# Optimization experiments

Hardware: AMD Instinct MI355X
Metric: run time of the kernel (lower is better)

The kernel has to match this reference:

```python
import jax, jax.numpy as jnp
import numpy as np


def setup_inputs() -> dict:
    key = jax.random.key(0)
    k1, k2 = jax.random.split(key)
    z = jax.random.normal(k1, (16, 256, 32, 32), dtype=jnp.float32)
    emb = jax.random.normal(k2, (8192, 256), dtype=jnp.float32)
    return {"z": z, "emb": emb}


def reference(z, emb):
    B, C, H, W = z.shape
    # [B,C,H,W] -> [B*H*W, C], distances in fp32 for precision
    z_f = jnp.transpose(z, (0, 2, 3, 1)).reshape(-1, C).astype(jnp.float32)
    e = emb.astype(jnp.float32)
    # squared-distance expansion: ||z||^2 - 2 z.e + ||e||^2  -> [N, K]
    d = (
        jnp.sum(z_f * z_f, axis=1, keepdims=True)
        - 2.0 * (z_f @ e.T)
        + jnp.sum(e * e, axis=1)[None, :]
    )
    idx = jnp.argmin(d, axis=1)  # [N]
    out = emb[idx].astype(z.dtype)  # codebook gather
    return jnp.transpose(out.reshape(B, H, W, C), (0, 3, 1, 2))
```

## Files before the change

kernel.cpp:

```cpp
#include <hip/hip_runtime.h>
#include <stdint.h>

#define NB   16
#define CD   256
#define HW   1024
#define NQ   16384
#define KCN  8192

typedef unsigned long long u64;
typedef unsigned short     u16;
using f32x4  = __attribute__((ext_vector_type(4))) float;
using bf16x8 = __attribute__((ext_vector_type(8))) __bf16;

#define ZTB_OFF  0
#define EMBB_OFF 8388608
#define EH_OFF   12582912
#define CAND_OFF 12615680

static __device__ __forceinline__ void gl_lds16(const void* g, void* l) {
  __builtin_amdgcn_global_load_lds(
      (const __attribute__((address_space(1))) void*)g,
      (__attribute__((address_space(3))) void*)l, 16, 0, 0);
}

static __device__ __forceinline__ unsigned bf16r(float x) {
  unsigned u = __float_as_uint(x);
  return (u + 0x7fffu + ((u >> 16) & 1u)) >> 16;
}

static __device__ __forceinline__ u64 umin64(u64 a, u64 b) { return a < b ? a : b; }
static __device__ __forceinline__ u64 umax64(u64 a, u64 b) { return a < b ? b : a; }

__global__ __launch_bounds__(256) void k_prep(const float* __restrict__ z,
                                              const float* __restrict__ emb,
                                              u16* __restrict__ zTb,
                                              u16* __restrict__ embB,
                                              float* __restrict__ eH) {
  const int bx = (int)blockIdx.x;
  if (bx < 1024) {
    __shared__ float tile[64][65];
    const int b   = bx >> 6;
    const int hwT = (bx >> 2) & 15;
    const int cT  = bx & 3;
    const int tx  = threadIdx.x & 63;
    const int ty  = threadIdx.x >> 6;
    const float* src = z + (size_t)(b * CD + cT * 64) * HW + hwT * 64;
#pragma unroll
    for (int i = 0; i < 16; ++i) {
      const int c_l = ty + 4 * i;
      tile[c_l][tx] = src[(size_t)c_l * HW + tx];
    }
    __syncthreads();
    const size_t dbase = (size_t)(b * HW + hwT * 64) * CD + cT * 64;
#pragma unroll
    for (int i = 0; i < 16; ++i) {
      const int hw_l = ty + 4 * i;
      zTb[dbase + (size_t)hw_l * CD + tx] = (u16)bf16r(tile[tx][hw_l]);
    }
  } else {
    const int wave = (bx - 1024) * 4 + ((int)threadIdx.x >> 6);
    const int lane = threadIdx.x & 63;
#pragma unroll
    for (int it = 0; it < 8; ++it) {
      const int row = wave * 8 + it;
      const float4 v = *(const float4*)(emb + (size_t)row * CD + lane * 4);
      uint2 pk;
      pk.x = bf16r(v.x) | (bf16r(v.y) << 16);
      pk.y = bf16r(v.z) | (bf16r(v.w) << 16);
      *(uint2*)(embB + (size_t)row * CD + lane * 4) = pk;
      float s = v.x * v.x + v.y * v.y + v.z * v.z + v.w * v.w;
#pragma unroll
      for (int off = 32; off; off >>= 1) s += __shfl_xor(s, off, 64);
      if (lane == 0) eH[row] = 0.5f * s + 1024.0f;
    }
  }
}


#define WAITV(N) asm volatile("s_waitcnt vmcnt(" #N ")" ::: "memory")
#define MEMFENCE() asm volatile("" ::: "memory")

__global__ __launch_bounds__(256, 2) void k_argmin(const u16* __restrict__ zTb,
                                                   const u16* __restrict__ embB,
                                                   const float* __restrict__ eH,
                                                   u64* __restrict__ cand) {
  __shared__ __align__(16) u16 Bs[4][128 * 64];

  const int tid  = (int)threadIdx.x;
  const int w    = tid >> 6;
  const int lane = tid & 63;
  const int l15  = lane & 15, quad = lane >> 4;
  const int q0    = (int)(blockIdx.x >> 3) * 128;
  const int split = (int)(blockIdx.x & 7);

  bf16x8 Af[2][4][2];
  {
    const char* aB = (const char*)zTb
                   + ((size_t)(q0 + w * 32 + l15) * CD + quad * 8) * 2;
#pragma unroll
    for (int i = 0; i < 2; ++i)
#pragma unroll
      for (int kc = 0; kc < 4; ++kc)
#pragma unroll
        for (int ks = 0; ks < 2; ++ks)
          Af[i][kc][ks] = *(const bf16x8*)(aB + i * 8192 + kc * 128 + ks * 64);
  }
  MEMFENCE();

  const char* bS = (const char*)embB + (size_t)split * (1024 * 512)
                 + (size_t)(w * 32 + (lane >> 3)) * 512
                 + (size_t)(((lane & 7) ^ (lane >> 3)) * 16);
  const int ldsW = w * 4096 + lane * 16;

#define STAGE(RING, NT_, KC_)                                                  \
  do {                                                                         \
    const char* _s = bS + (NT_) * 65536 + (KC_) * 128;                         \
    char* _d = (char*)Bs[RING] + ldsW;                                         \
    gl_lds16(_s,         _d);                                                  \
    gl_lds16(_s + 4096,  _d + 1024);                                           \
    gl_lds16(_s + 8192,  _d + 2048);                                           \
    gl_lds16(_s + 12288, _d + 3072);                                           \
  } while (0)

  const int bR0 = l15 * 128 + ((quad ^ (l15 & 7)) * 16);
  const int bR1 = bR0 ^ 64;

  f32x4 acc[2][8];
  float b1[8][2], b2[8][2];
  const float FMAX = __uint_as_float(0x7F7FFFFFu);
#pragma unroll
  for (int s = 0; s < 8; ++s) { b1[s][0] = b1[s][1] = FMAX; b2[s][0] = b2[s][1] = FMAX; }

  STAGE(0, 0, 0); MEMFENCE();
  STAGE(1, 0, 1); MEMFENCE();
  STAGE(2, 0, 2); MEMFENCE();

#define MFMA_INT(RING, KC_)                                                    \
  do {                                                                         \
    const char* _b = (const char*)Bs[RING];                                    \
    _Pragma("unroll")                                                          \
    for (int ks = 0; ks < 2; ++ks) {                                           \
      bf16x8 bfr[8];                                                           \
      const int _o = ks ? bR1 : bR0;                                           \
      _Pragma("unroll")                                                        \
      for (int j = 0; j < 8; ++j)                                              \
        bfr[j] = *(const bf16x8*)(_b + j * 2048 + _o);                         \
      __builtin_amdgcn_s_setprio(1);                                           \
      _Pragma("unroll")                                                        \
      for (int i = 0; i < 2; ++i)                                              \
        _Pragma("unroll")                                                      \
        for (int j = 0; j < 8; ++j)                                            \
          acc[i][j] = __builtin_amdgcn_mfma_f32_16x16x32_bf16(                 \
              Af[i][KC_][ks], bfr[j], acc[i][j], 0, 0, 0);                     \
      __builtin_amdgcn_s_setprio(0);                                           \
    }                                                                          \
  } while (0)

#define EPILOGUE(NT_)                                                          \
  do {                                                                         \
    _Pragma("unroll")                                                          \
    for (int i = 0; i < 2; ++i)                                                \
      _Pragma("unroll")                                                        \
      for (int r = 0; r < 4; ++r) {                                            \
        const int s = i * 4 + r;                                               \
        float kq[8];                                                           \
        _Pragma("unroll")                                                      \
        for (int j = 0; j < 8; ++j)                                            \
          kq[j] = __uint_as_float(                                             \
              (__float_as_uint(eh[j] - acc[i][j][r]) & ~63u)                   \
              | (unsigned)((NT_) * 8 + j));                                    \
        _Pragma("unroll")                                                      \
        for (int h = 0; h < 2; ++h) {                                          \
          const float k0 = kq[4 * h], k1 = kq[4 * h + 1];                      \
          const float k2 = kq[4 * h + 2], k3 = kq[4 * h + 3];                  \
          const float lo01 = fminf(k0, k1), hi01 = fmaxf(k0, k1);              \
          const float lo23 = fminf(k2, k3), hi23 = fmaxf(k2, k3);              \
          const float best = fminf(lo01, lo23);                                \
          const float sec  = fminf(fmaxf(lo01, lo23), fminf(hi01, hi23));      \
          b2[s][h] = fminf(fmaxf(best, b1[s][h]), fminf(sec, b2[s][h]));       \
          b1[s][h] = fminf(best, b1[s][h]);                                    \
        }                                                                      \
      }                                                                        \
  } while (0)

  float eh[8];

  for (int nt = 0; nt < 7; ++nt) {
    const int n0 = split * 1024 + nt * 128;
#pragma unroll
    for (int i = 0; i < 2; ++i)
#pragma unroll
      for (int j = 0; j < 8; ++j) acc[i][j] = f32x4{0.f, 0.f, 0.f, 0.f};

    WAITV(8); __builtin_amdgcn_s_barrier(); MEMFENCE();
    STAGE(3, nt, 3); MEMFENCE();
#pragma unroll
    for (int j = 0; j < 8; ++j) eh[j] = eH[n0 + j * 16 + l15];
    MEMFENCE();
    MFMA_INT(0, 0);
    WAITV(16); __builtin_amdgcn_s_barrier(); MEMFENCE();
    STAGE(0, nt + 1, 0); MEMFENCE();
    MFMA_INT(1, 1);
    WAITV(16); __builtin_amdgcn_s_barrier(); MEMFENCE();
    STAGE(1, nt + 1, 1); MEMFENCE();
    MFMA_INT(2, 2);
    WAITV(16); __builtin_amdgcn_s_barrier(); MEMFENCE();
    STAGE(2, nt + 1, 2); MEMFENCE();
    MFMA_INT(3, 3);

    EPILOGUE(nt);
  }

  {
    const int n0 = split * 1024 + 7 * 128;
#pragma unroll
    for (int i = 0; i < 2; ++i)
#pragma unroll
      for (int j = 0; j < 8; ++j) acc[i][j] = f32x4{0.f, 0.f, 0.f, 0.f};

    WAITV(8); __builtin_amdgcn_s_barrier(); MEMFENCE();
    STAGE(3, 7, 3); MEMFENCE();
#pragma unroll
    for (int j = 0; j < 8; ++j) eh[j] = eH[n0 + j * 16 + l15];
    MEMFENCE();
    MFMA_INT(0, 0);

    WAITV(16); __builtin_amdgcn_s_barrier(); MEMFENCE();
    MFMA_INT(1, 1);

    WAITV(12); __builtin_amdgcn_s_barrier(); MEMFENCE();
    MFMA_INT(2, 2);

    WAITV(8); __builtin_amdgcn_s_barrier(); MEMFENCE();
    MFMA_INT(3, 3);

    EPILOGUE(7);
  }
#undef STAGE
#undef MFMA_INT
#undef EPILOGUE

  const int wh = w >> 1;
#pragma unroll
  for (int s = 0; s < 8; ++s) {
#pragma unroll
    for (int h = 0; h < 2; ++h) {
      u64 x1 = ((u64)__float_as_uint(b1[s][h]) << 32) | (unsigned)l15;
      u64 x2 = ((u64)__float_as_uint(b2[s][h]) << 32) | (unsigned)l15;
#pragma unroll
      for (int off = 1; off < 16; off <<= 1) {
        const u64 o1 = __shfl_xor(x1, off, 64);
        const u64 o2 = __shfl_xor(x2, off, 64);
        const u64 lo = umin64(x1, o1);
        const u64 hi = umax64(x1, o1);
        x1 = lo;
        x2 = umin64(hi, umin64(x2, o2));
      }
      if (l15 == 0) {
        const int i = s >> 2, r = s & 3;
        const int q = q0 + w * 32 + i * 16 + quad * 4 + r;
        const unsigned kb1 = (unsigned)(x1 >> 32), kb2 = (unsigned)(x2 >> 32);
        const int n1 = split * 1024 + (int)((kb1 >> 3) & 7) * 128
                       + (int)(kb1 & 7) * 16 + (int)(x1 & 15);
        const int n2 = split * 1024 + (int)((kb2 >> 3) & 7) * 128
                       + (int)(kb2 & 7) * 16 + (int)(x2 & 15);
        cand[(size_t)q * 32 + split * 4 + h * 2 + 0] = ((u64)kb1 << 32) | (unsigned)n1;
        cand[(size_t)q * 32 + split * 4 + h * 2 + 1] = ((u64)kb2 << 32) | (unsigned)n2;
      }
    }
  }
}

__global__ __launch_bounds__(256) void k_pick_out(const float* __restrict__ z,
                                                  const float* __restrict__ emb,
                                                  const u64* __restrict__ cand,
                                                  float* __restrict__ out) {
  __shared__ float zs[64][256];
  const int t    = (int)threadIdx.x;
  const int lane = t & 63;
  const int wv   = t >> 6;
  const int sub  = lane >> 4;
  const int l15  = lane & 15;
  const int q0b  = (int)blockIdx.x * 64;
  const int b    = q0b >> 10, hw0 = q0b & 1023;

  {
    const float* zb = z + ((size_t)(b * CD + wv * 64)) * HW + hw0;
    const int sw = lane & 31;
#pragma unroll 8
    for (int i = 0; i < 64; ++i) {
      const float v = zb[(size_t)i * HW + lane];
      zs[lane][(wv * 64 + i) ^ sw] = v;
    }
  }
  __syncthreads();

  float keep[4][16];
#pragma unroll
  for (int it = 0; it < 4; ++it) {
    const int hwl = wv * 16 + it * 4 + sub;
    const int q   = q0b + hwl;

    const u64* cp = cand + (size_t)q * 32 + l15 * 2;
    const u64 v0 = cp[0], v1 = cp[1];
    u64 s0 = umin64(v0, v1), s1 = umax64(v0, v1), s2 = ~0ull, s3 = ~0ull;
#pragma unroll
    for (int off = 1; off < 16; off <<= 1) {
      const u64 b0 = __shfl_xor(s0, off, 64);
      const u64 b1 = __shfl_xor(s1, off, 64);
      const u64 b2 = __shfl_xor(s2, off, 64);
      const u64 b3 = __shfl_xor(s3, off, 64);
      const u64 c0 = umin64(s0, b0);
      const u64 c1 = umin64(umin64(s1, b1), umax64(s0, b0));
      const u64 c2 = umin64(umin64(s2, b2),
                            umin64(umax64(s1, b0), umax64(s0, b1)));
      const u64 c3 = umin64(umin64(umin64(s3, b3), umax64(s2, b0)),
                            umin64(umax64(s0, b2), umax64(s1, b1)));
      s0 = c0; s1 = c1; s2 = c2; s3 = c3;
    }
    const u64 sel[4] = {s0, s1, s2, s3};

    const int swq = hwl & 31;
    float zq[16];
#pragma unroll
    for (int j = 0; j < 16; ++j) zq[j] = zs[hwl][(j * 16 + l15) ^ swq];

    double bd = 1e300;
    int bi = 0x7fffffff;
#pragma unroll
    for (int j = 0; j < 16; ++j) keep[it][j] = 0.f;
#pragma unroll
    for (int c4 = 0; c4 < 4; ++c4) {
      const int idx = (int)(unsigned)(sel[c4] & 0xffffffffull);
      const float* er = emb + (size_t)idx * CD;
      float ev[16];
#pragma unroll
      for (int j = 0; j < 16; ++j) ev[j] = er[j * 16 + l15];
      double s = 0.0;
#pragma unroll
      for (int j = 0; j < 16; ++j) {
        const double d = (double)zq[j] - (double)ev[j];
        s += d * d;
      }
#pragma unroll
      for (int off = 1; off < 16; off <<= 1) s += __shfl_xor(s, off, 64);
      const bool better = (s < bd) || (s == bd && idx < bi);
      if (better) {
        bd = s; bi = idx;
#pragma unroll
        for (int j = 0; j < 16; ++j) keep[it][j] = ev[j];
      }
    }
  }

  __syncthreads();
#pragma unroll
  for (int it = 0; it < 4; ++it) {
    const int hwl = wv * 16 + it * 4 + sub;
    const int swq = hwl & 31;
#pragma unroll
    for (int j = 0; j < 16; ++j) zs[hwl][(j * 16 + l15) ^ swq] = keep[it][j];
  }
  __syncthreads();
  {
    float* ob = out + ((size_t)(b * CD + wv * 64)) * HW + hw0;
    const int sw = lane & 31;
#pragma unroll 8
    for (int i = 0; i < 64; ++i)
      ob[(size_t)i * HW + lane] = zs[lane][(wv * 64 + i) ^ sw];
  }
}

extern "C" void kernel_launch(void* const* d_in, const int* in_sizes, int n_in,
                              void* d_out, int out_size, void* d_ws, size_t ws_size,
                              hipStream_t stream) {
  const float* z   = (const float*)d_in[0];
  const float* emb = (const float*)d_in[1];
  float* out = (float*)d_out;

  char* ws = (char*)d_ws;
  u16*   zTb  = (u16*)(ws + ZTB_OFF);
  u16*   embB = (u16*)(ws + EMBB_OFF);
  float* eH   = (float*)(ws + EH_OFF);
  u64*   cand = (u64*)(ws + CAND_OFF);

  k_prep<<<1280, 256, 0, stream>>>(z, emb, zTb, embB, eH);
  k_argmin<<<1024, 256, 0, stream>>>(zTb, embB, eH, cand);
  k_pick_out<<<256, 256, 0, stream>>>(z, emb, cand, out);
}
```

Baseline: 182.4 us.

## Use three-slot rotating LDS ring in argmin and widen pick-out blocks

The argmin kernel's B-tile staging drops from a four-slot ring with fixed slot-to-k-chunk mapping to a three-slot ring with rotating pointers. This cuts LDS use, which may allow higher occupancy, at the cost of a shallower prefetch depth and retuned vmcnt waits. The pick-out kernel now runs 1024 threads per block, so each 16-lane group handles one query instead of four serial iterations per wave. That exposes more parallelism for the candidate re-scoring and the gather latency.

```diff
diff --git a/kernel.cpp b/kernel.cpp
--- a/kernel.cpp
+++ b/kernel.cpp
@@ -84,7 +84,7 @@
                                                    const u16* __restrict__ embB,
                                                    const float* __restrict__ eH,
                                                    u64* __restrict__ cand) {
-  __shared__ __align__(16) u16 Bs[4][128 * 64];
+  __shared__ __align__(16) u16 Bs[3][128 * 64];
 
   const int tid  = (int)threadIdx.x;
   const int w    = tid >> 6;
@@ -112,10 +112,10 @@
                  + (size_t)(((lane & 7) ^ (lane >> 3)) * 16);
   const int ldsW = w * 4096 + lane * 16;
 
-#define STAGE(RING, NT_, KC_)                                                  \
+#define STAGEP(P_, NT_, KC_)                                                   \
   do {                                                                         \
     const char* _s = bS + (NT_) * 65536 + (KC_) * 128;                         \
-    char* _d = (char*)Bs[RING] + ldsW;                                         \
+    char* _d = (char*)(P_) + ldsW;                                             \
     gl_lds16(_s,         _d);                                                  \
     gl_lds16(_s + 4096,  _d + 1024);                                           \
     gl_lds16(_s + 8192,  _d + 2048);                                           \
@@ -131,13 +131,16 @@
 #pragma unroll
   for (int s = 0; s < 8; ++s) { b1[s][0] = b1[s][1] = FMAX; b2[s][0] = b2[s][1] = FMAX; }
 
-  STAGE(0, 0, 0); MEMFENCE();
-  STAGE(1, 0, 1); MEMFENCE();
-  STAGE(2, 0, 2); MEMFENCE();
-
-#define MFMA_INT(RING, KC_)                                                    \
+  char* p0 = (char*)Bs[0];
+  char* p1 = (char*)Bs[1];
+  char* p2 = (char*)Bs[2];
+
+  STAGEP(p0, 0, 0); MEMFENCE();
+  STAGEP(p1, 0, 1); MEMFENCE();
+
+#define MFMA_P(P_, KC_)                                                        \
   do {                                                                         \
-    const char* _b = (const char*)Bs[RING];                                    \
+    const char* _b = (const char*)(P_);                                        \
     _Pragma("unroll")                                                          \
     for (int ks = 0; ks < 2; ++ks) {                                           \
       bf16x8 bfr[8];                                                           \
@@ -192,23 +195,28 @@
 #pragma unroll
       for (int j = 0; j < 8; ++j) acc[i][j] = f32x4{0.f, 0.f, 0.f, 0.f};
 
-    WAITV(8); __builtin_amdgcn_s_barrier(); MEMFENCE();
-    STAGE(3, nt, 3); MEMFENCE();
+    WAITV(4); __builtin_amdgcn_s_barrier(); MEMFENCE();
+    STAGEP(p2, nt, 2); MEMFENCE();
 #pragma unroll
     for (int j = 0; j < 8; ++j) eh[j] = eH[n0 + j * 16 + l15];
     MEMFENCE();
-    MFMA_INT(0, 0);
-    WAITV(16); __builtin_amdgcn_s_barrier(); MEMFENCE();
-    STAGE(0, nt + 1, 0); MEMFENCE();
-    MFMA_INT(1, 1);
-    WAITV(16); __builtin_amdgcn_s_barrier(); MEMFENCE();
-    STAGE(1, nt + 1, 1); MEMFENCE();
-    MFMA_INT(2, 2);
-    WAITV(16); __builtin_amdgcn_s_barrier(); MEMFENCE();
-    STAGE(2, nt + 1, 2); MEMFENCE();
-    MFMA_INT(3, 3);
+    MFMA_P(p0, 0);
+
+    WAITV(12); __builtin_amdgcn_s_barrier(); MEMFENCE();
+    STAGEP(p0, nt, 3); MEMFENCE();
+    MFMA_P(p1, 1);
+
+    WAITV(12); __builtin_amdgcn_s_barrier(); MEMFENCE();
+    STAGEP(p1, nt + 1, 0); MEMFENCE();
+    MFMA_P(p2, 2);
+
+    WAITV(4); __builtin_amdgcn_s_barrier(); MEMFENCE();
+    STAGEP(p2, nt + 1, 1); MEMFENCE();
+    MFMA_P(p0, 3);
 
     EPILOGUE(nt);
+
+    char* tmp = p0; p0 = p1; p1 = p2; p2 = tmp;
   }
 
   {
@@ -218,29 +226,29 @@
 #pragma unroll
       for (int j = 0; j < 8; ++j) acc[i][j] = f32x4{0.f, 0.f, 0.f, 0.f};
 
-    WAITV(8); __builtin_amdgcn_s_barrier(); MEMFENCE();
-    STAGE(3, 7, 3); MEMFENCE();
+    WAITV(4); __builtin_amdgcn_s_barrier(); MEMFENCE();
+    STAGEP(p2, 7, 2); MEMFENCE();
 #pragma unroll
     for (int j = 0; j < 8; ++j) eh[j] = eH[n0 + j * 16 + l15];
     MEMFENCE();
-    MFMA_INT(0, 0);
-
-    WAITV(16); __builtin_amdgcn_s_barrier(); MEMFENCE();
-    MFMA_INT(1, 1);
+    MFMA_P(p0, 0);
 
     WAITV(12); __builtin_amdgcn_s_barrier(); MEMFENCE();
-    MFMA_INT(2, 2);
-
-    WAITV(8); __builtin_amdgcn_s_barrier(); MEMFENCE();
-    MFMA_INT(3, 3);
+    STAGEP(p0, 7, 3); MEMFENCE();
+    MFMA_P(p1, 1);
+
+    WAITV(12); __builtin_amdgcn_s_barrier(); MEMFENCE();
+    MFMA_P(p2, 2);
+
+    WAITV(0); __builtin_amdgcn_s_barrier(); MEMFENCE();
+    MFMA_P(p0, 3);
 
     EPILOGUE(7);
   }
-#undef STAGE
-#undef MFMA_INT
+#undef STAGEP
+#undef MFMA_P
 #undef EPILOGUE
 
-  const int wh = w >> 1;
 #pragma unroll
   for (int s = 0; s < 8; ++s) {
 #pragma unroll
@@ -271,103 +279,91 @@
   }
 }
 
-__global__ __launch_bounds__(256) void k_pick_out(const float* __restrict__ z,
-                                                  const float* __restrict__ emb,
-                                                  const u64* __restrict__ cand,
-                                                  float* __restrict__ out) {
+__global__ __launch_bounds__(1024) void k_pick_out(const float* __restrict__ z,
+                                                   const float* __restrict__ emb,
+                                                   const u64* __restrict__ cand,
+                                                   float* __restrict__ out) {
   __shared__ float zs[64][256];
   const int t    = (int)threadIdx.x;
   const int lane = t & 63;
   const int wv   = t >> 6;
-  const int sub  = lane >> 4;
-  const int l15  = lane & 15;
+  const int l15  = t & 15;
+  const int g    = t >> 4;
   const int q0b  = (int)blockIdx.x * 64;
   const int b    = q0b >> 10, hw0 = q0b & 1023;
 
   {
-    const float* zb = z + ((size_t)(b * CD + wv * 64)) * HW + hw0;
+    const float* zb = z + ((size_t)(b * CD + wv * 16)) * HW + hw0;
     const int sw = lane & 31;
-#pragma unroll 8
-    for (int i = 0; i < 64; ++i) {
-      const float v = zb[(size_t)i * HW + lane];
-      zs[lane][(wv * 64 + i) ^ sw] = v;
-    }
+#pragma unroll
+    for (int i = 0; i < 16; ++i)
+      zs[lane][(wv * 16 + i) ^ sw] = zb[(size_t)i * HW + lane];
   }
   __syncthreads();
 
-  float keep[4][16];
-#pragma unroll
-  for (int it = 0; it < 4; ++it) {
-    const int hwl = wv * 16 + it * 4 + sub;
-    const int q   = q0b + hwl;
-
-    const u64* cp = cand + (size_t)q * 32 + l15 * 2;
-    const u64 v0 = cp[0], v1 = cp[1];
-    u64 s0 = umin64(v0, v1), s1 = umax64(v0, v1), s2 = ~0ull, s3 = ~0ull;
-#pragma unroll
-    for (int off = 1; off < 16; off <<= 1) {
-      const u64 b0 = __shfl_xor(s0, off, 64);
-      const u64 b1 = __shfl_xor(s1, off, 64);
-      const u64 b2 = __shfl_xor(s2, off, 64);
-      const u64 b3 = __shfl_xor(s3, off, 64);
-      const u64 c0 = umin64(s0, b0);
-      const u64 c1 = umin64(umin64(s1, b1), umax64(s0, b0));
-      const u64 c2 = umin64(umin64(s2, b2),
-                            umin64(umax64(s1, b0), umax64(s0, b1)));
-      const u64 c3 = umin64(umin64(umin64(s3, b3), umax64(s2, b0)),
-                            umin64(umax64(s0, b2), umax64(s1, b1)));
-      s0 = c0; s1 = c1; s2 = c2; s3 = c3;
-    }
-    const u64 sel[4] = {s0, s1, s2, s3};
-
-    const int swq = hwl & 31;
-    float zq[16];
-#pragma unroll
-    for (int j = 0; j < 16; ++j) zq[j] = zs[hwl][(j * 16 + l15) ^ swq];
-
-    double bd = 1e300;
-    int bi = 0x7fffffff;
-#pragma unroll
-    for (int j = 0; j < 16; ++j) keep[it][j] = 0.f;
-#pragma unroll
-    for (int c4 = 0; c4 < 4; ++c4) {
-      const int idx = (int)(unsigned)(sel[c4] & 0xffffffffull);
-      const float* er = emb + (size_t)idx * CD;
-      float ev[16];
-#pragma unroll
-      for (int j = 0; j < 16; ++j) ev[j] = er[j * 16 + l15];
-      double s = 0.0;
-#pragma unroll
-      for (int j = 0; j < 16; ++j) {
-        const double d = (double)zq[j] - (double)ev[j];
-        s += d * d;
-      }
-#pragma unroll
-      for (int off = 1; off < 16; off <<= 1) s += __shfl_xor(s, off, 64);
-      const bool better = (s < bd) || (s == bd && idx < bi);
-      if (better) {
-        bd = s; bi = idx;
-#pragma unroll
-        for (int j = 0; j < 16; ++j) keep[it][j] = ev[j];
-      }
+  const int q = q0b + g;
+  const u64* cp = cand + (size_t)q * 32 + l15 * 2;
+  const u64 v0 = cp[0], v1 = cp[1];
+  u64 s0 = umin64(v0, v1), s1 = umax64(v0, v1), s2 = ~0ull, s3 = ~0ull;
+#pragma unroll
+  for (int off = 1; off < 16; off <<= 1) {
+    const u64 b0 = __shfl_xor(s0, off, 64);
+    const u64 b1 = __shfl_xor(s1, off, 64);
+    const u64 b2 = __shfl_xor(s2, off, 64);
+    const u64 b3 = __shfl_xor(s3, off, 64);
+    const u64 c0 = umin64(s0, b0);
+    const u64 c1 = umin64(umin64(s1, b1), umax64(s0, b0));
+    const u64 c2 = umin64(umin64(s2, b2),
+                          umin64(umax64(s1, b0), umax64(s0, b1)));
+    const u64 c3 = umin64(umin64(umin64(s3, b3), umax64(s2, b0)),
+                          umin64(umax64(s0, b2), umax64(s1, b1)));
+    s0 = c0; s1 = c1; s2 = c2; s3 = c3;
+  }
+  const u64 sel[4] = {s0, s1, s2, s3};
+
+  const int swq = g & 31;
+  float zq[16];
+#pragma unroll
+  for (int j = 0; j < 16; ++j) zq[j] = zs[g][(j * 16 + l15) ^ swq];
+
+  double bd = 1e300;
+  int bi = 0x7fffffff;
+  float keep[16];
+#pragma unroll
+  for (int j = 0; j < 16; ++j) keep[j] = 0.f;
+#pragma unroll
+  for (int c4 = 0; c4 < 4; ++c4) {
+    const int idx = (int)(unsigned)(sel[c4] & 0xffffffffull);
+    const float* er = emb + (size_t)idx * CD;
+    float ev[16];
+#pragma unroll
+    for (int j = 0; j < 16; ++j) ev[j] = er[j * 16 + l15];
+    double s = 0.0;
+#pragma unroll
+    for (int j = 0; j < 16; ++j) {
+      const double d = (double)zq[j] - (double)ev[j];
+      s += d * d;
+    }
+#pragma unroll
+    for (int off = 1; off < 16; off <<= 1) s += __shfl_xor(s, off, 64);
+    const bool better = (s < bd) || (s == bd && idx < bi);
+    if (better) {
+      bd = s; bi = idx;
+#pragma unroll
+      for (int j = 0; j < 16; ++j) keep[j] = ev[j];
     }
   }
 
   __syncthreads();
 #pragma unroll
-  for (int it = 0; it < 4; ++it) {
-    const int hwl = wv * 16 + it * 4 + sub;
-    const int swq = hwl & 31;
-#pragma unroll
-    for (int j = 0; j < 16; ++j) zs[hwl][(j * 16 + l15) ^ swq] = keep[it][j];
-  }
+  for (int j = 0; j < 16; ++j) zs[g][(j * 16 + l15) ^ swq] = keep[j];
   __syncthreads();
   {
-    float* ob = out + ((size_t)(b * CD + wv * 64)) * HW + hw0;
+    float* ob = out + ((size_t)(b * CD + wv * 16)) * HW + hw0;
     const int sw = lane & 31;
-#pragma unroll 8
-    for (int i = 0; i < 64; ++i)
-      ob[(size_t)i * HW + lane] = zs[lane][(wv * 64 + i) ^ sw];
+#pragma unroll
+    for (int i = 0; i < 16; ++i)
+      ob[(size_t)i * HW + lane] = zs[lane][(wv * 16 + i) ^ sw];
   }
 }
 
@@ -386,5 +382,5 @@
 
   k_prep<<<1280, 256, 0, stream>>>(z, emb, zTb, embB, eH);
   k_argmin<<<1024, 256, 0, stream>>>(zTb, embB, eH, cand);
-  k_pick_out<<<256, 256, 0, stream>>>(z, emb, cand, out);
-}
+  k_pick_out<<<256, 1024, 0, stream>>>(z, emb, cand, out);
+}
```

After: 175.0 us. 1.04x faster.

## Widen pick_out to 1024 threads and vectorize zTb stores in prep

Applied to the files above, without the earlier changes.

k_prep's transposed bf16 write now packs four channels into one ushort4 store instead of scalar u16 stores. k_pick_out is restructured to 1024-thread blocks with one 16-lane group per query, replacing the loop over four queries per group. The kept winner vector in registers is replaced by re-reading the winning embedding row from global memory. LDS is laid out as [256][66] with float2 loads and stores. This aims to raise parallelism and cut register pressure in the rerank stage, at the cost of an extra embedding-row read and a different LDS bank pattern.

```diff
diff --git a/kernel.cpp b/kernel.cpp
--- a/kernel.cpp
+++ b/kernel.cpp
@@ -52,10 +52,17 @@
     }
     __syncthreads();
     const size_t dbase = (size_t)(b * HW + hwT * 64) * CD + cT * 64;
-#pragma unroll
-    for (int i = 0; i < 16; ++i) {
-      const int hw_l = ty + 4 * i;
-      zTb[dbase + (size_t)hw_l * CD + tx] = (u16)bf16r(tile[tx][hw_l]);
+    const int rsub = tx >> 4;
+    const int cq   = (tx & 15) * 4;
+#pragma unroll
+    for (int i = 0; i < 4; ++i) {
+      const int r = ty * 16 + i * 4 + rsub;
+      ushort4 pk;
+      pk.x = (u16)bf16r(tile[cq + 0][r]);
+      pk.y = (u16)bf16r(tile[cq + 1][r]);
+      pk.z = (u16)bf16r(tile[cq + 2][r]);
+      pk.w = (u16)bf16r(tile[cq + 3][r]);
+      *(ushort4*)(zTb + dbase + (size_t)r * CD + cq) = pk;
     }
   } else {
     const int wave = (bx - 1024) * 4 + ((int)threadIdx.x >> 6);
@@ -240,7 +247,6 @@
 #undef MFMA_INT
 #undef EPILOGUE
 
-  const int wh = w >> 1;
 #pragma unroll
   for (int s = 0; s < 8; ++s) {
 #pragma unroll
@@ -271,103 +277,89 @@
   }
 }
 
-__global__ __launch_bounds__(256) void k_pick_out(const float* __restrict__ z,
-                                                  const float* __restrict__ emb,
-                                                  const u64* __restrict__ cand,
-                                                  float* __restrict__ out) {
-  __shared__ float zs[64][256];
+__global__ __launch_bounds__(1024) void k_pick_out(const float* __restrict__ z,
+                                                   const float* __restrict__ emb,
+                                                   const u64* __restrict__ cand,
+                                                   float* __restrict__ out) {
+  __shared__ float zs[256][66];
   const int t    = (int)threadIdx.x;
   const int lane = t & 63;
   const int wv   = t >> 6;
-  const int sub  = lane >> 4;
-  const int l15  = lane & 15;
+  const int l15  = t & 15;
+  const int g    = t >> 4;
   const int q0b  = (int)blockIdx.x * 64;
   const int b    = q0b >> 10, hw0 = q0b & 1023;
 
   {
-    const float* zb = z + ((size_t)(b * CD + wv * 64)) * HW + hw0;
-    const int sw = lane & 31;
-#pragma unroll 8
-    for (int i = 0; i < 64; ++i) {
-      const float v = zb[(size_t)i * HW + lane];
-      zs[lane][(wv * 64 + i) ^ sw] = v;
+    const int hw   = (lane & 31) * 2;
+    const int csub = lane >> 5;
+#pragma unroll
+    for (int i = 0; i < 8; ++i) {
+      const int c = wv * 16 + i * 2 + csub;
+      const float2 v = *(const float2*)(z + ((size_t)(b * CD + c)) * HW + hw0 + hw);
+      *(float2*)&zs[c][hw] = v;
     }
   }
   __syncthreads();
 
-  float keep[4][16];
-#pragma unroll
-  for (int it = 0; it < 4; ++it) {
-    const int hwl = wv * 16 + it * 4 + sub;
-    const int q   = q0b + hwl;
-
-    const u64* cp = cand + (size_t)q * 32 + l15 * 2;
-    const u64 v0 = cp[0], v1 = cp[1];
-    u64 s0 = umin64(v0, v1), s1 = umax64(v0, v1), s2 = ~0ull, s3 = ~0ull;
-#pragma unroll
-    for (int off = 1; off < 16; off <<= 1) {
-      const u64 b0 = __shfl_xor(s0, off, 64);
-      const u64 b1 = __shfl_xor(s1, off, 64);
-      const u64 b2 = __shfl_xor(s2, off, 64);
-      const u64 b3 = __shfl_xor(s3, off, 64);
-      const u64 c0 = umin64(s0, b0);
-      const u64 c1 = umin64(umin64(s1, b1), umax64(s0, b0));
-      const u64 c2 = umin64(umin64(s2, b2),
-                            umin64(umax64(s1, b0), umax64(s0, b1)));
-      const u64 c3 = umin64(umin64(umin64(s3, b3), umax64(s2, b0)),
-                            umin64(umax64(s0, b2), umax64(s1, b1)));
-      s0 = c0; s1 = c1; s2 = c2; s3 = c3;
-    }
-    const u64 sel[4] = {s0, s1, s2, s3};
-
-    const int swq = hwl & 31;
-    float zq[16];
-#pragma unroll
-    for (int j = 0; j < 16; ++j) zq[j] = zs[hwl][(j * 16 + l15) ^ swq];
-
-    double bd = 1e300;
-    int bi = 0x7fffffff;
-#pragma unroll
-    for (int j = 0; j < 16; ++j) keep[it][j] = 0.f;
-#pragma unroll
-    for (int c4 = 0; c4 < 4; ++c4) {
-      const int idx = (int)(unsigned)(sel[c4] & 0xffffffffull);
-      const float* er = emb + (size_t)idx * CD;
-      float ev[16];
-#pragma unroll
-      for (int j = 0; j < 16; ++j) ev[j] = er[j * 16 + l15];
-      double s = 0.0;
-#pragma unroll
-      for (int j = 0; j < 16; ++j) {
-        const double d = (double)zq[j] - (double)ev[j];
-        s += d * d;
-      }
-#pragma unroll
-      for (int off = 1; off < 16; off <<= 1) s += __shfl_xor(s, off, 64);
-      const bool better = (s < bd) || (s == bd && idx < bi);
-      if (better) {
-        bd = s; bi = idx;
-#pragma unroll
-        for (int j = 0; j < 16; ++j) keep[it][j] = ev[j];
-      }
-    }
+  const int q = q0b + g;
+  const u64* cp = cand + (size_t)q * 32 + l15 * 2;
+  const u64 v0 = cp[0], v1 = cp[1];
+  u64 s0 = umin64(v0, v1), s1 = umax64(v0, v1), s2 = ~0ull, s3 = ~0ull;
+#pragma unroll
+  for (int off = 1; off < 16; off <<= 1) {
+    const u64 b0 = __shfl_xor(s0, off, 64);
+    const u64 b1 = __shfl_xor(s1, off, 64);
+    const u64 b2 = __shfl_xor(s2, off, 64);
+    const u64 b3 = __shfl_xor(s3, off, 64);
+    const u64 c0 = umin64(s0, b0);
+    const u64 c1 = umin64(umin64(s1, b1), umax64(s0, b0));
+    const u64 c2 = umin64(umin64(s2, b2),
+                          umin64(umax64(s1, b0), umax64(s0, b1)));
+    const u64 c3 = umin64(umin64(umin64(s3, b3), umax64(s2, b0)),
+                          umin64(umax64(s0, b2), umax64(s1, b1)));
+    s0 = c0; s1 = c1; s2 = c2; s3 = c3;
+  }
+  const u64 sel[4] = {s0, s1, s2, s3};
+
+  float zq[16];
+#pragma unroll
+  for (int j = 0; j < 16; ++j) zq[j] = zs[j * 16 + l15][g];
+
+  double bd = 1e300;
+  int bi = 0x7fffffff;
+#pragma unroll
+  for (int c4 = 0; c4 < 4; ++c4) {
+    const int idx = (int)(unsigned)(sel[c4] & 0xffffffffull);
+    const float* er = emb + (size_t)idx * CD;
+    double s = 0.0;
+#pragma unroll
+    for (int j = 0; j < 16; ++j) {
+      const double d = (double)zq[j] - (double)er[j * 16 + l15];
+      s += d * d;
+    }
+#pragma unroll
+    for (int off = 1; off < 16; off <<= 1) s += __shfl_xor(s, off, 64);
+    const bool better = (s < bd) || (s == bd && idx < bi);
+    if (better) { bd = s; bi = idx; }
   }
 
   __syncthreads();
-#pragma unroll
-  for (int it = 0; it < 4; ++it) {
-    const int hwl = wv * 16 + it * 4 + sub;
-    const int swq = hwl & 31;
-#pragma unroll
-    for (int j = 0; j < 16; ++j) zs[hwl][(j * 16 + l15) ^ swq] = keep[it][j];
+  {
+    const float* ew = emb + (size_t)bi * CD;
+#pragma unroll
+    for (int j = 0; j < 16; ++j) zs[j * 16 + l15][g] = ew[j * 16 + l15];
   }
   __syncthreads();
   {
-    float* ob = out + ((size_t)(b * CD + wv * 64)) * HW + hw0;
-    const int sw = lane & 31;
-#pragma unroll 8
-    for (int i = 0; i < 64; ++i)
-      ob[(size_t)i * HW + lane] = zs[lane][(wv * 64 + i) ^ sw];
+    const int hw   = (lane & 31) * 2;
+    const int csub = lane >> 5;
+#pragma unroll
+    for (int i = 0; i < 8; ++i) {
+      const int c = wv * 16 + i * 2 + csub;
+      const float2 v = *(const float2*)&zs[c][hw];
+      *(float2*)(out + ((size_t)(b * CD + c)) * HW + hw0 + hw) = v;
+    }
   }
 }
 
@@ -386,5 +378,5 @@
 
   k_prep<<<1280, 256, 0, stream>>>(z, emb, zTb, embB, eH);
   k_argmin<<<1024, 256, 0, stream>>>(zTb, embB, eH, cand);
-  k_pick_out<<<256, 256, 0, stream>>>(z, emb, cand, out);
-}
+  k_pick_out<<<256, 1024, 0, stream>>>(z, emb, cand, out);
+}
```

New measurement: 172.1 us. 5.6% less time.
